# Optimization experiments

Hardware: AMD Instinct MI355X
Metric: run time of the kernel (lower is better)

The kernel has to match this reference:

```python
import jax, jax.numpy as jnp
import numpy as np
from jax import lax

BN_EPS = 1e-5


def _batchnorm(x, gamma, beta):
    # training-mode BatchNorm2d: batch stats over (B, T, J), biased variance
    mean = jnp.mean(x, axis=(0, 2, 3), keepdims=True)
    var = jnp.var(x, axis=(0, 2, 3), keepdims=True)
    inv = lax.rsqrt(var + BN_EPS)
    return (x - mean) * inv * gamma[None, :, None, None] + beta[None, :, None, None]


def setup_inputs() -> dict:
    key = jax.random.key(0)
    ks = jax.random.split(key, 6)
    B, C, T, J = 32, 64, 300, 25
    Cout, K = 64, 9
    x = jax.random.normal(ks[0], (B, C, T, J), dtype=jnp.float32)
    A = jax.random.uniform(ks[1], (J, J), dtype=jnp.float32)
    gcn_w = jax.random.normal(ks[2], (Cout, C), dtype=jnp.float32) * (1.0 / np.sqrt(C))
    gcn_b = jax.random.normal(ks[3], (Cout,), dtype=jnp.float32) * 0.01
    tcn_w = jax.random.normal(ks[4], (Cout, Cout, K, 1), dtype=jnp.float32) * (1.0 / np.sqrt(Cout * K))
    tcn_b = jax.random.normal(ks[5], (Cout,), dtype=jnp.float32) * 0.01
    return {
        "x": x, "A": A,
        "gcn_w": gcn_w, "gcn_b": gcn_b,
        "bn1_g": jnp.ones((Cout,), jnp.float32), "bn1_b": jnp.zeros((Cout,), jnp.float32),
        "tcn_w": tcn_w, "tcn_b": tcn_b,
        "bn2_g": jnp.ones((Cout,), jnp.float32), "bn2_b": jnp.zeros((Cout,), jnp.float32),
    }


def reference(x, A, gcn_w, gcn_b, bn1_g, bn1_b, tcn_w, tcn_b, bn2_g, bn2_b):
    # x: [B, C, T, J]; A: [J, J]
    res = x  # identity residual (in_channels == out_channels, stride == 1)
    # spatial graph conv: joint mixing then 1x1 channel mix (Conv2d k=1)
    y = jnp.einsum('bctj,jk->bctk', x, A)
    y = jnp.einsum('bctj,oc->botj', y, gcn_w) + gcn_b[None, :, None, None]
    y = _batchnorm(y, bn1_g, bn1_b)
    # temporal conv: ReLU -> Conv2d((K,1), pad (K//2,0)) -> BN
    y = jax.nn.relu(y)
    K = tcn_w.shape[2]
    y = lax.conv_general_dilated(
        y, tcn_w, window_strides=(1, 1), padding=((K // 2, K // 2), (0, 0)),
        dimension_numbers=('NCHW', 'OIHW', 'NCHW'))
    y = y + tcn_b[None, :, None, None]
    y = _batchnorm(y, bn2_g, bn2_b)
    return jax.nn.relu(y + res)
```

## Files before the change

kernel.cpp:

```cpp
#include <hip/hip_runtime.h>

#define B_   32
#define C_   64
#define T_   300
#define J_   25
#define K9   9
constexpr int PLANE = T_ * J_;
constexpr int BCTJ  = B_ * C_ * PLANE;
constexpr float BN_EPS = 1e-5f;
constexpr float BN_N   = (float)(B_ * T_ * J_);

typedef __attribute__((ext_vector_type(8))) _Float16 f16x8;
typedef __attribute__((ext_vector_type(2))) _Float16 f16x2;
typedef __attribute__((ext_vector_type(4))) float f32x4;
typedef __attribute__((ext_vector_type(8))) unsigned short u16x8;
typedef __attribute__((ext_vector_type(4))) unsigned short u16x4;

__device__ inline unsigned short f2h(float f) {
  _Float16 h = (_Float16)f;
  return __builtin_bit_cast(unsigned short, h);
}
__device__ inline float h2f(unsigned short u) {
  return (float)__builtin_bit_cast(_Float16, u);
}

__device__ inline void gload16(const unsigned short* g, unsigned short* l) {
  __builtin_amdgcn_global_load_lds(
      (const __attribute__((address_space(1))) unsigned int*)g,
      (__attribute__((address_space(3))) unsigned int*)l, 16, 0, 0);
}

__global__ __launch_bounds__(256) void prep_kernel(const float* __restrict__ tw,
                                                   const float* __restrict__ gw,
                                                   const float* __restrict__ A,
                                                   unsigned short* __restrict__ Wb,
                                                   unsigned short* __restrict__ Gb,
                                                   unsigned short* __restrict__ AdT) {
  int idx = blockIdx.x * 256 + threadIdx.x;
  if (idx < C_ * C_ * K9) {
    int o = idx / (C_ * K9);
    int rem = idx % (C_ * K9);
    int c = rem / K9, kt = rem % K9;
    Wb[kt * (C_ * C_) + o * C_ + c] = f2h(tw[idx]);
  } else if (idx < C_ * C_ * K9 + C_ * C_) {
    int i = idx - C_ * C_ * K9;
    Gb[i] = f2h(gw[i]);
  } else if (idx < C_ * C_ * K9 + C_ * C_ + 256 * 256) {
    int i = idx - (C_ * C_ * K9 + C_ * C_);
    int n = i >> 8, m = i & 255;
    float v = 0.f;
    if (n < 250 && m < 250) {
      if (n / 25 == m / 25) v = A[(m % 25) * 25 + (n % 25)];
    }
    AdT[i] = f2h(v);
  }
}

constexpr int TTG = 10;
__global__ __launch_bounds__(256, 4) void gcn_mfma_kernel(
    const float* __restrict__ x, const unsigned short* __restrict__ AdT,
    const unsigned short* __restrict__ Gb, const float* __restrict__ gbias,
    unsigned short* __restrict__ y1Tb, float* __restrict__ part1) {
  __shared__ unsigned short Xs[C_ * 256];
  __shared__ float sred[4][64], qred[4][64];
  int bid = (blockIdx.x & 7) * 120 + (blockIdx.x >> 3);
  int b = bid / (T_ / TTG), tile = bid % (T_ / TTG);
  int t0 = tile * TTG;
  int tid = threadIdx.x;

  {
    size_t sbase = (size_t)b * (C_ * PLANE) + (size_t)t0 * J_;
    int c0 = tid >> 6;
    int m  = (tid & 63) * 4;
    float4 vb[16];
#pragma unroll
    for (int k = 0; k < 16; ++k) {
      size_t off = sbase + (size_t)(c0 + 4 * k) * PLANE + m;
      size_t offc = off > (size_t)(BCTJ - 4) ? (size_t)(BCTJ - 4) : off;
      float4 v = *(const float4*)(x + offc);
      if (off != offc) {
        v.x = v.z; v.y = v.w; v.z = 0.f; v.w = 0.f;
      }
      vb[k] = v;
    }
#pragma unroll
    for (int k = 0; k < 16; ++k) {
      int c = c0 + 4 * k;
      unsigned p0 = (unsigned)f2h(vb[k].x) | ((unsigned)f2h(vb[k].y) << 16);
      unsigned p1 = (unsigned)f2h(vb[k].z) | ((unsigned)f2h(vb[k].w) << 16);
      int elem = ((c << 8) | m) ^ ((c & 7) << 3);
      *(uint2*)&Xs[elem] = make_uint2(p0, p1);
    }
  }
  __syncthreads();

  int l = tid & 63, w = tid >> 6;
  int lr = l & 15, lh = l >> 4;
  int n0 = w * 64;

  f32x4 acc1[4][4];
#pragma unroll
  for (int mf = 0; mf < 4; ++mf)
#pragma unroll
    for (int nf = 0; nf < 4; ++nf) acc1[mf][nf] = (f32x4)0.f;

  int qminw = ((n0 / 25) * 25) >> 5;
  int qmaxw = min(7, ((((n0 + 63) / 25) + 1) * 25 - 1) >> 5);
  for (int q = qminw; q <= qmaxw; ++q) {
    f16x8 afx[4];
#pragma unroll
    for (int mf = 0; mf < 4; ++mf) {
      int c = mf * 16 + lr;
      int elem = ((c << 8) | (q * 32 + lh * 8)) ^ ((c & 7) << 3);
      afx[mf] = *(const f16x8*)&Xs[elem];
    }
#pragma unroll
    for (int nf = 0; nf < 4; ++nf) {
      int nbase = n0 + nf * 16;
      int ql = ((nbase / 25) * 25) >> 5;
      int qh = min(7, ((((nbase + 15) / 25) + 1) * 25 - 1) >> 5);
      if (q < ql || q > qh) continue;
      int n = nbase + lr;
      f16x8 bfx = *(const f16x8*)&AdT[n * 256 + q * 32 + lh * 8];
#pragma unroll
      for (int mf = 0; mf < 4; ++mf)
        acc1[mf][nf] = __builtin_amdgcn_mfma_f32_16x16x32_f16(afx[mf], bfx, acc1[mf][nf], 0, 0, 0);
    }
  }
  __syncthreads();

#pragma unroll
  for (int mf = 0; mf < 4; ++mf) {
    int cb = mf * 16 + 4 * lh;
#pragma unroll
    for (int nf = 0; nf < 4; ++nf) {
      int n = n0 + nf * 16 + lr;
      unsigned p0 = (unsigned)f2h(acc1[mf][nf][0]) | ((unsigned)f2h(acc1[mf][nf][1]) << 16);
      unsigned p1 = (unsigned)f2h(acc1[mf][nf][2]) | ((unsigned)f2h(acc1[mf][nf][3]) << 16);
      int e0 = ((n << 6) | cb) ^ ((n & 7) << 3);
      *(uint2*)&Xs[e0] = make_uint2(p0, p1);
    }
  }
  __syncthreads();

  f32x4 acc[4][4];
#pragma unroll
  for (int mf = 0; mf < 4; ++mf)
#pragma unroll
    for (int nf = 0; nf < 4; ++nf) acc[mf][nf] = (f32x4)0.f;

  f16x8 af[4][2];
#pragma unroll
  for (int mf = 0; mf < 4; ++mf) {
    const unsigned short* wp = Gb + (mf * 16 + lr) * C_ + lh * 8;
    af[mf][0] = *(const f16x8*)(wp);
    af[mf][1] = *(const f16x8*)(wp + 32);
  }
  f16x8 bfr[4][2];
#pragma unroll
  for (int nf = 0; nf < 4; ++nf) {
    int r = n0 + nf * 16 + lr;
    int sw = (r & 7) << 3;
    bfr[nf][0] = *(const f16x8*)&Xs[((r << 6) | (lh * 8)) ^ sw];
    bfr[nf][1] = *(const f16x8*)&Xs[((r << 6) | (32 + lh * 8)) ^ sw];
  }
#pragma unroll
  for (int mf = 0; mf < 4; ++mf)
#pragma unroll
    for (int nf = 0; nf < 4; ++nf) {
      acc[mf][nf] = __builtin_amdgcn_mfma_f32_16x16x32_f16(af[mf][0], bfr[nf][0], acc[mf][nf], 0, 0, 0);
      acc[mf][nf] = __builtin_amdgcn_mfma_f32_16x16x32_f16(af[mf][1], bfr[nf][1], acc[mf][nf], 0, 0, 0);
    }
  __syncthreads();

#pragma unroll
  for (int mf = 0; mf < 4; ++mf) {
    float4 gb4 = *(const float4*)(gbias + mf * 16 + 4 * lh);
    int cb = mf * 16 + 4 * lh;
    float sv[4] = {0.f, 0.f, 0.f, 0.f}, qv[4] = {0.f, 0.f, 0.f, 0.f};
#pragma unroll
    for (int nf = 0; nf < 4; ++nf) {
      int n = n0 + nf * 16 + lr;
      float v0 = acc[mf][nf][0] + gb4.x;
      float v1 = acc[mf][nf][1] + gb4.y;
      float v2 = acc[mf][nf][2] + gb4.z;
      float v3 = acc[mf][nf][3] + gb4.w;
      if (n < 250) {
        sv[0] += v0; qv[0] += v0 * v0;
        sv[1] += v1; qv[1] += v1 * v1;
        sv[2] += v2; qv[2] += v2 * v2;
        sv[3] += v3; qv[3] += v3 * v3;
      }
      unsigned p0 = (unsigned)f2h(v0) | ((unsigned)f2h(v1) << 16);
      unsigned p1 = (unsigned)f2h(v2) | ((unsigned)f2h(v3) << 16);
      int e0 = ((n << 6) | cb) ^ ((n & 7) << 3);
      *(uint2*)&Xs[e0] = make_uint2(p0, p1);
    }
#pragma unroll
    for (int reg = 0; reg < 4; ++reg) {
      float s = sv[reg], q = qv[reg];
#pragma unroll
      for (int m = 1; m < 16; m <<= 1) {
        s += __shfl_xor(s, m);
        q += __shfl_xor(q, m);
      }
      if (lr == 0) {
        int o = mf * 16 + 4 * lh + reg;
        sred[w][o] = s; qred[w][o] = q;
      }
    }
  }
  __syncthreads();

  unsigned short* ydst = y1Tb + ((size_t)b * PLANE + (size_t)t0 * J_) * C_;
#pragma unroll
  for (int it = 0; it < 8; ++it) {
    int task = it * 256 + tid;
    int n = task >> 3, ch = task & 7;
    if (n < 250) {
      int e = ((n << 6) | (ch * 8)) ^ ((n & 7) << 3);
      u16x8 v = *(const u16x8*)&Xs[e];
      *(u16x8*)(ydst + (size_t)n * C_ + ch * 8) = v;
    }
  }
  if (tid < 64) {
    float S = 0.f, Q = 0.f;
#pragma unroll
    for (int i = 0; i < 4; ++i) { S += sred[i][tid]; Q += qred[i][tid]; }
    part1[bid * 128 + tid] = S;
    part1[bid * 128 + 64 + tid] = Q;
  }
}

__global__ __launch_bounds__(256) void bnparam_reduce_kernel(
    const float* __restrict__ part, int nparts,
    const float* __restrict__ g, const float* __restrict__ b,
    float* __restrict__ bnp, unsigned short* __restrict__ bnph) {
  int c = blockIdx.x;
  int tid = threadIdx.x;
  float S = 0.f, Q = 0.f;
  for (int k = tid; k < nparts; k += 256) {
    S += part[k * 128 + c];
    Q += part[k * 128 + 64 + c];
  }
#pragma unroll
  for (int off = 32; off > 0; off >>= 1) {
    S += __shfl_down(S, off);
    Q += __shfl_down(Q, off);
  }
  __shared__ float ls[2][4];
  int wv = tid >> 6, ln = tid & 63;
  if (ln == 0) { ls[0][wv] = S; ls[1][wv] = Q; }
  __syncthreads();
  if (tid == 0) {
    float St = ls[0][0] + ls[0][1] + ls[0][2] + ls[0][3];
    float Qt = ls[1][0] + ls[1][1] + ls[1][2] + ls[1][3];
    float mean = St / BN_N;
    float var = Qt / BN_N - mean * mean;
    float inv = rsqrtf(var + BN_EPS);
    float sc = g[c] * inv;
    float sh = b[c] - mean * sc;
    bnp[c] = sc;
    bnp[C_ + c] = sh;
    bnph[c] = f2h(sc);
    bnph[C_ + c] = f2h(sh);
  }
}

constexpr int TT = 10;
constexpr int ZROWS_TOT = 456;
__global__ __launch_bounds__(256, 2) void tcn_mfma_kernel(
    const unsigned short* __restrict__ y1Tb, const unsigned short* __restrict__ Wb,
    const unsigned short* __restrict__ bnph1, const float* __restrict__ tbias,
    unsigned short* __restrict__ y2b, float* __restrict__ part2) {
  __shared__ unsigned short zs[ZROWS_TOT * C_];
  __shared__ float sred[4][64], qred[4][64];
  unsigned short* zs2 = zs;
  int bid = (blockIdx.x & 7) * 120 + (blockIdx.x >> 3);
  int b = bid / (T_ / TT), tile = bid % (T_ / TT);
  int t0 = tile * TT;
  int tid = threadIdx.x;
  int g0 = t0 * J_ - 100;

  {
    const unsigned short* bb = y1Tb + (size_t)b * PLANE * C_;
#pragma unroll
    for (int k = 0; k < 15; ++k) {
      int P = k * 256 + tid;
      if (P < 3600) {
        int r = P >> 3, p = P & 7;
        int gr = g0 + r;
        int grc = min(max(gr, 0), PLANE - 1);
        const unsigned short* src = bb + (size_t)grc * C_ + ((p ^ (r & 7)) << 3);
        int ldsoff = (k * 256 + (tid & 192)) << 4;
        gload16(src, (unsigned short*)((char*)zs + ldsoff));
      }
    }
  }

  int l = tid & 63, w = tid >> 6;
  int lr = l & 15, lh = l >> 4;
  int n0 = w * 64;

  f16x2 scA[4], shA[4], scB[4], shB[4];
  {
    const f16x2* scp = (const f16x2*)(bnph1);
    const f16x2* shp = (const f16x2*)(bnph1 + C_);
#pragma unroll
    for (int i = 0; i < 4; ++i) {
      scA[i] = scp[lh * 4 + i];      shA[i] = shp[lh * 4 + i];
      scB[i] = scp[16 + lh * 4 + i]; shB[i] = shp[16 + lh * 4 + i];
    }
  }
  f16x2 z2 = (f16x2)((_Float16)0.f);

  f32x4 acc[4][4];
#pragma unroll
  for (int mf = 0; mf < 4; ++mf)
#pragma unroll
    for (int nf = 0; nf < 4; ++nf) acc[mf][nf] = (f32x4)0.f;

  f16x8 afc[4][2];
#pragma unroll
  for (int mf = 0; mf < 4; ++mf) {
    const unsigned short* wp = Wb + (mf * 16 + lr) * C_ + lh * 8;
    afc[mf][0] = *(const f16x8*)(wp);
    afc[mf][1] = *(const f16x8*)(wp + 32);
  }
  __syncthreads();

  auto load_bfr = [&](int kt, f16x8 out[4][2]) {
#pragma unroll
    for (int nf = 0; nf < 4; ++nf) {
      int r = n0 + nf * 16 + lr + 25 * kt;
      int gr = g0 + r;
      int sw = (r & 7) << 3;
      uint4 ra = *(const uint4*)&zs[((r << 6) | (lh * 8)) ^ sw];
      uint4 rb = *(const uint4*)&zs[((r << 6) | (32 + lh * 8)) ^ sw];
      f16x2 a0 = __builtin_bit_cast(f16x2, ra.x);
      f16x2 a1 = __builtin_bit_cast(f16x2, ra.y);
      f16x2 a2 = __builtin_bit_cast(f16x2, ra.z);
      f16x2 a3 = __builtin_bit_cast(f16x2, ra.w);
      f16x2 b0 = __builtin_bit_cast(f16x2, rb.x);
      f16x2 b1 = __builtin_bit_cast(f16x2, rb.y);
      f16x2 b2 = __builtin_bit_cast(f16x2, rb.z);
      f16x2 b3 = __builtin_bit_cast(f16x2, rb.w);
      a0 = __builtin_elementwise_max(a0 * scA[0] + shA[0], z2);
      a1 = __builtin_elementwise_max(a1 * scA[1] + shA[1], z2);
      a2 = __builtin_elementwise_max(a2 * scA[2] + shA[2], z2);
      a3 = __builtin_elementwise_max(a3 * scA[3] + shA[3], z2);
      b0 = __builtin_elementwise_max(b0 * scB[0] + shB[0], z2);
      b1 = __builtin_elementwise_max(b1 * scB[1] + shB[1], z2);
      b2 = __builtin_elementwise_max(b2 * scB[2] + shB[2], z2);
      b3 = __builtin_elementwise_max(b3 * scB[3] + shB[3], z2);
      unsigned m = ((unsigned)gr < (unsigned)PLANE && r < 450) ? 0xFFFFFFFFu : 0u;
      uint4 pa, pb;
      pa.x = __builtin_bit_cast(unsigned int, a0) & m;
      pa.y = __builtin_bit_cast(unsigned int, a1) & m;
      pa.z = __builtin_bit_cast(unsigned int, a2) & m;
      pa.w = __builtin_bit_cast(unsigned int, a3) & m;
      pb.x = __builtin_bit_cast(unsigned int, b0) & m;
      pb.y = __builtin_bit_cast(unsigned int, b1) & m;
      pb.z = __builtin_bit_cast(unsigned int, b2) & m;
      pb.w = __builtin_bit_cast(unsigned int, b3) & m;
      out[nf][0] = __builtin_bit_cast(f16x8, pa);
      out[nf][1] = __builtin_bit_cast(f16x8, pb);
    }
  };

  f16x8 bcur[4][2], bnxt[4][2];
  load_bfr(0, bcur);

#pragma unroll
  for (int kt = 0; kt < K9; ++kt) {
    f16x8 afn[4][2];
    if (kt < K9 - 1) {
#pragma unroll
      for (int mf = 0; mf < 4; ++mf) {
        const unsigned short* wp = Wb + (kt + 1) * (C_ * C_) + (mf * 16 + lr) * C_ + lh * 8;
        afn[mf][0] = *(const f16x8*)(wp);
        afn[mf][1] = *(const f16x8*)(wp + 32);
      }
      load_bfr(kt + 1, bnxt);
    }
    __builtin_amdgcn_s_setprio(1);
#pragma unroll
    for (int mf = 0; mf < 4; ++mf)
#pragma unroll
      for (int nf = 0; nf < 4; ++nf) {
        acc[mf][nf] = __builtin_amdgcn_mfma_f32_16x16x32_f16(afc[mf][0], bcur[nf][0], acc[mf][nf], 0, 0, 0);
        acc[mf][nf] = __builtin_amdgcn_mfma_f32_16x16x32_f16(afc[mf][1], bcur[nf][1], acc[mf][nf], 0, 0, 0);
      }
    __builtin_amdgcn_s_setprio(0);
    if (kt < K9 - 1) {
#pragma unroll
      for (int mf = 0; mf < 4; ++mf) {
        afc[mf][0] = afn[mf][0];
        afc[mf][1] = afn[mf][1];
      }
#pragma unroll
      for (int nf = 0; nf < 4; ++nf) {
        bcur[nf][0] = bnxt[nf][0];
        bcur[nf][1] = bnxt[nf][1];
      }
    }
  }
  __syncthreads();

#pragma unroll
  for (int mf = 0; mf < 4; ++mf) {
    float4 tb4 = *(const float4*)(tbias + mf * 16 + 4 * lh);
    float sv[4] = {0.f, 0.f, 0.f, 0.f}, qv[4] = {0.f, 0.f, 0.f, 0.f};
#pragma unroll
    for (int nf = 0; nf < 4; ++nf) {
      int n = n0 + nf * 16 + lr;
      if (n < 250) {
#pragma unroll
        for (int reg = 0; reg < 4; ++reg) {
          int o = mf * 16 + 4 * lh + reg;
          float v = acc[mf][nf][reg] + ((const float*)&tb4)[reg];
          zs2[o * 260 + n] = f2h(v);
          sv[reg] += v; qv[reg] += v * v;
        }
      }
    }
#pragma unroll
    for (int reg = 0; reg < 4; ++reg) {
      float s = sv[reg], q = qv[reg];
#pragma unroll
      for (int m = 1; m < 16; m <<= 1) {
        s += __shfl_xor(s, m);
        q += __shfl_xor(q, m);
      }
      if (lr == 0) {
        int o = mf * 16 + 4 * lh + reg;
        sred[w][o] = s; qred[w][o] = q;
      }
    }
  }
  __syncthreads();

  unsigned short* ydst = y2b + (size_t)b * (C_ * PLANE) + (size_t)t0 * J_;
#pragma unroll
  for (int it = 0; it < 32; ++it) {
    int task = it * 256 + tid;
    if (task < 8000) {
      int o = task / 125;
      int k = task - o * 125;
      unsigned d = *(const unsigned*)&zs2[o * 260 + 2 * k];
      *(unsigned*)(ydst + (size_t)o * PLANE + 2 * k) = d;
    }
  }
  if (tid < 64) {
    float S = 0.f, Q = 0.f;
#pragma unroll
    for (int i = 0; i < 4; ++i) { S += sred[i][tid]; Q += qred[i][tid]; }
    part2[bid * 128 + tid] = S;
    part2[bid * 128 + 64 + tid] = Q;
  }
}

__global__ __launch_bounds__(256) void final_kernel(const unsigned short* __restrict__ y2b,
                                                    const float* __restrict__ x,
                                                    const float* __restrict__ bnp2,
                                                    float* __restrict__ out) {
  int lb = (blockIdx.x & 7) * 1875 + (blockIdx.x >> 3);
  int i = lb * 256 + threadIdx.x;
  if (i >= BCTJ / 4) return;
  int c = (i / (PLANE / 4)) & (C_ - 1);
  float sc = bnp2[c], sh = bnp2[C_ + c];
  u16x4 yv = *(const u16x4*)(y2b + (size_t)i * 4);
  float4 xv = ((const float4*)x)[i];
  float4 v;
  v.x = fmaxf(fmaf(h2f(yv[0]), sc, sh) + xv.x, 0.f);
  v.y = fmaxf(fmaf(h2f(yv[1]), sc, sh) + xv.y, 0.f);
  v.z = fmaxf(fmaf(h2f(yv[2]), sc, sh) + xv.z, 0.f);
  v.w = fmaxf(fmaf(h2f(yv[3]), sc, sh) + xv.w, 0.f);
  ((float4*)out)[i] = v;
}

extern "C" void kernel_launch(void* const* d_in, const int* in_sizes, int n_in,
                              void* d_out, int out_size, void* d_ws, size_t ws_size,
                              hipStream_t stream) {
  const float* x     = (const float*)d_in[0];
  const float* A     = (const float*)d_in[1];
  const float* gcn_w = (const float*)d_in[2];
  const float* gcn_b = (const float*)d_in[3];
  const float* bn1_g = (const float*)d_in[4];
  const float* bn1_b = (const float*)d_in[5];
  const float* tcn_w = (const float*)d_in[6];
  const float* tcn_b = (const float*)d_in[7];
  const float* bn2_g = (const float*)d_in[8];
  const float* bn2_b = (const float*)d_in[9];
  float* out = (float*)d_out;

  unsigned short* y1Tb = (unsigned short*)d_ws;
  unsigned short* y2b  = y1Tb + BCTJ;
  unsigned short* Wb   = y2b + BCTJ;
  unsigned short* Gb   = Wb + C_ * C_ * K9;
  unsigned short* AdT  = Gb + C_ * C_;
  unsigned short* bnph = AdT + 256 * 256;
  float* part = (float*)(bnph + 256);
  float* bnp  = part + 960 * 128;

  int prep_n = C_ * C_ * K9 + C_ * C_ + 256 * 256;
  prep_kernel<<<(prep_n + 255) / 256, 256, 0, stream>>>(tcn_w, gcn_w, A, Wb, Gb, AdT);
  gcn_mfma_kernel<<<B_ * (T_ / TTG), 256, 0, stream>>>(x, AdT, Gb, gcn_b, y1Tb, part);
  bnparam_reduce_kernel<<<64, 256, 0, stream>>>(part, B_ * (T_ / TTG), bn1_g, bn1_b, bnp, bnph);
  tcn_mfma_kernel<<<B_ * (T_ / TT), 256, 0, stream>>>(y1Tb, Wb, bnph, tcn_b, y2b, part);
  bnparam_reduce_kernel<<<64, 256, 0, stream>>>(part, B_ * (T_ / TT), bn2_g, bn2_b, bnp + 128, bnph + 128);
  final_kernel<<<BCTJ / 4 / 256, 256, 0, stream>>>(y2b, x, bnp + 128, out);
}
```

Before: 118.2 us.

## Tile temporal conv per (batch, joint) and store intermediate channel-last with transposing final kernel

The temporal conv kernel now processes one full time sequence per (batch, joint) block, 800 blocks, instead of 10-timestep tiles spanning all joints. This cuts the halo rows loaded per block and shrinks LDS so three blocks fit per CU. The per-k B-fragment prefetch is dropped, and the intermediate is written channel-last through a padded LDS tile. The final kernel now transposes that layout through shared memory back to NCHW before the BN, residual and ReLU step. The trade-offs are gathered 128-byte row loads with stride J*C, uneven work across waves, and an extra LDS transpose in the final pass.

```diff
diff --git a/kernel.cpp b/kernel.cpp
--- a/kernel.cpp
+++ b/kernel.cpp
@@ -267,31 +267,28 @@
   }
 }
 
-constexpr int TT = 10;
-constexpr int ZROWS_TOT = 456;
-__global__ __launch_bounds__(256, 2) void tcn_mfma_kernel(
+constexpr int ZRJ = 312;
+__global__ __launch_bounds__(256, 3) void tcn_mfma_kernel(
     const unsigned short* __restrict__ y1Tb, const unsigned short* __restrict__ Wb,
     const unsigned short* __restrict__ bnph1, const float* __restrict__ tbias,
-    unsigned short* __restrict__ y2b, float* __restrict__ part2) {
-  __shared__ unsigned short zs[ZROWS_TOT * C_];
+    unsigned short* __restrict__ y2T, float* __restrict__ part2) {
+  __shared__ __align__(16) unsigned short zsU[304 * 72];
   __shared__ float sred[4][64], qred[4][64];
-  unsigned short* zs2 = zs;
-  int bid = (blockIdx.x & 7) * 120 + (blockIdx.x >> 3);
-  int b = bid / (T_ / TT), tile = bid % (T_ / TT);
-  int t0 = tile * TT;
+  unsigned short* zs  = zsU;
+  unsigned short* zs2 = zsU;
+  int bid = (blockIdx.x & 7) * 100 + (blockIdx.x >> 3);
+  int b = bid / J_, j = bid % J_;
   int tid = threadIdx.x;
-  int g0 = t0 * J_ - 100;
 
   {
     const unsigned short* bb = y1Tb + (size_t)b * PLANE * C_;
 #pragma unroll
-    for (int k = 0; k < 15; ++k) {
+    for (int k = 0; k < 10; ++k) {
       int P = k * 256 + tid;
-      if (P < 3600) {
+      if (P < ZRJ * 8) {
         int r = P >> 3, p = P & 7;
-        int gr = g0 + r;
-        int grc = min(max(gr, 0), PLANE - 1);
-        const unsigned short* src = bb + (size_t)grc * C_ + ((p ^ (r & 7)) << 3);
+        int tc = min(max(r - 4, 0), T_ - 1);
+        const unsigned short* src = bb + (size_t)(tc * J_ + j) * C_ + ((p ^ (r & 7)) << 3);
         int ldsoff = (k * 256 + (tid & 192)) << 4;
         gload16(src, (unsigned short*)((char*)zs + ldsoff));
       }
@@ -300,7 +297,8 @@
 
   int l = tid & 63, w = tid >> 6;
   int lr = l & 15, lh = l >> 4;
-  int n0 = w * 64;
+  int n0 = w * 80;
+  int nfmax = (w < 3) ? 5 : 4;
 
   f16x2 scA[4], shA[4], scB[4], shB[4];
   {
@@ -314,11 +312,11 @@
   }
   f16x2 z2 = (f16x2)((_Float16)0.f);
 
-  f32x4 acc[4][4];
+  f32x4 acc[4][5];
 #pragma unroll
   for (int mf = 0; mf < 4; ++mf)
 #pragma unroll
-    for (int nf = 0; nf < 4; ++nf) acc[mf][nf] = (f32x4)0.f;
+    for (int nf = 0; nf < 5; ++nf) acc[mf][nf] = (f32x4)0.f;
 
   f16x8 afc[4][2];
 #pragma unroll
@@ -329,11 +327,22 @@
   }
   __syncthreads();
 
-  auto load_bfr = [&](int kt, f16x8 out[4][2]) {
-#pragma unroll
-    for (int nf = 0; nf < 4; ++nf) {
-      int r = n0 + nf * 16 + lr + 25 * kt;
-      int gr = g0 + r;
+#pragma unroll
+  for (int kt = 0; kt < K9; ++kt) {
+    f16x8 afn[4][2];
+    if (kt < K9 - 1) {
+#pragma unroll
+      for (int mf = 0; mf < 4; ++mf) {
+        const unsigned short* wp = Wb + (kt + 1) * (C_ * C_) + (mf * 16 + lr) * C_ + lh * 8;
+        afn[mf][0] = *(const f16x8*)(wp);
+        afn[mf][1] = *(const f16x8*)(wp + 32);
+      }
+    }
+    f16x8 bfr[5][2];
+#pragma unroll
+    for (int nf = 0; nf < 5; ++nf) {
+      if (nf >= nfmax) continue;
+      int r = n0 + nf * 16 + lr + kt;
       int sw = (r & 7) << 3;
       uint4 ra = *(const uint4*)&zs[((r << 6) | (lh * 8)) ^ sw];
       uint4 rb = *(const uint4*)&zs[((r << 6) | (32 + lh * 8)) ^ sw];
@@ -353,7 +362,7 @@
       b1 = __builtin_elementwise_max(b1 * scB[1] + shB[1], z2);
       b2 = __builtin_elementwise_max(b2 * scB[2] + shB[2], z2);
       b3 = __builtin_elementwise_max(b3 * scB[3] + shB[3], z2);
-      unsigned m = ((unsigned)gr < (unsigned)PLANE && r < 450) ? 0xFFFFFFFFu : 0u;
+      unsigned m = ((unsigned)(r - 4) < (unsigned)T_) ? 0xFFFFFFFFu : 0u;
       uint4 pa, pb;
       pa.x = __builtin_bit_cast(unsigned int, a0) & m;
       pa.y = __builtin_bit_cast(unsigned int, a1) & m;
@@ -363,33 +372,17 @@
       pb.y = __builtin_bit_cast(unsigned int, b1) & m;
       pb.z = __builtin_bit_cast(unsigned int, b2) & m;
       pb.w = __builtin_bit_cast(unsigned int, b3) & m;
-      out[nf][0] = __builtin_bit_cast(f16x8, pa);
-      out[nf][1] = __builtin_bit_cast(f16x8, pb);
-    }
-  };
-
-  f16x8 bcur[4][2], bnxt[4][2];
-  load_bfr(0, bcur);
-
-#pragma unroll
-  for (int kt = 0; kt < K9; ++kt) {
-    f16x8 afn[4][2];
-    if (kt < K9 - 1) {
-#pragma unroll
-      for (int mf = 0; mf < 4; ++mf) {
-        const unsigned short* wp = Wb + (kt + 1) * (C_ * C_) + (mf * 16 + lr) * C_ + lh * 8;
-        afn[mf][0] = *(const f16x8*)(wp);
-        afn[mf][1] = *(const f16x8*)(wp + 32);
-      }
-      load_bfr(kt + 1, bnxt);
+      bfr[nf][0] = __builtin_bit_cast(f16x8, pa);
+      bfr[nf][1] = __builtin_bit_cast(f16x8, pb);
     }
     __builtin_amdgcn_s_setprio(1);
 #pragma unroll
     for (int mf = 0; mf < 4; ++mf)
 #pragma unroll
-      for (int nf = 0; nf < 4; ++nf) {
-        acc[mf][nf] = __builtin_amdgcn_mfma_f32_16x16x32_f16(afc[mf][0], bcur[nf][0], acc[mf][nf], 0, 0, 0);
-        acc[mf][nf] = __builtin_amdgcn_mfma_f32_16x16x32_f16(afc[mf][1], bcur[nf][1], acc[mf][nf], 0, 0, 0);
+      for (int nf = 0; nf < 5; ++nf) {
+        if (nf >= nfmax) continue;
+        acc[mf][nf] = __builtin_amdgcn_mfma_f32_16x16x32_f16(afc[mf][0], bfr[nf][0], acc[mf][nf], 0, 0, 0);
+        acc[mf][nf] = __builtin_amdgcn_mfma_f32_16x16x32_f16(afc[mf][1], bfr[nf][1], acc[mf][nf], 0, 0, 0);
       }
     __builtin_amdgcn_s_setprio(0);
     if (kt < K9 - 1) {
@@ -398,11 +391,6 @@
         afc[mf][0] = afn[mf][0];
         afc[mf][1] = afn[mf][1];
       }
-#pragma unroll
-      for (int nf = 0; nf < 4; ++nf) {
-        bcur[nf][0] = bnxt[nf][0];
-        bcur[nf][1] = bnxt[nf][1];
-      }
     }
   }
   __syncthreads();
@@ -412,16 +400,21 @@
     float4 tb4 = *(const float4*)(tbias + mf * 16 + 4 * lh);
     float sv[4] = {0.f, 0.f, 0.f, 0.f}, qv[4] = {0.f, 0.f, 0.f, 0.f};
 #pragma unroll
-    for (int nf = 0; nf < 4; ++nf) {
-      int n = n0 + nf * 16 + lr;
-      if (n < 250) {
-#pragma unroll
-        for (int reg = 0; reg < 4; ++reg) {
-          int o = mf * 16 + 4 * lh + reg;
-          float v = acc[mf][nf][reg] + ((const float*)&tb4)[reg];
-          zs2[o * 260 + n] = f2h(v);
-          sv[reg] += v; qv[reg] += v * v;
-        }
+    for (int nf = 0; nf < 5; ++nf) {
+      if (nf >= nfmax) continue;
+      int t = n0 + nf * 16 + lr;
+      if (t < T_) {
+        float v0 = acc[mf][nf][0] + tb4.x;
+        float v1 = acc[mf][nf][1] + tb4.y;
+        float v2 = acc[mf][nf][2] + tb4.z;
+        float v3 = acc[mf][nf][3] + tb4.w;
+        sv[0] += v0; qv[0] += v0 * v0;
+        sv[1] += v1; qv[1] += v1 * v1;
+        sv[2] += v2; qv[2] += v2 * v2;
+        sv[3] += v3; qv[3] += v3 * v3;
+        unsigned p0 = (unsigned)f2h(v0) | ((unsigned)f2h(v1) << 16);
+        unsigned p1 = (unsigned)f2h(v2) | ((unsigned)f2h(v3) << 16);
+        *(uint2*)&zs2[t * 72 + mf * 16 + 4 * lh] = make_uint2(p0, p1);
       }
     }
 #pragma unroll
@@ -440,15 +433,14 @@
   }
   __syncthreads();
 
-  unsigned short* ydst = y2b + (size_t)b * (C_ * PLANE) + (size_t)t0 * J_;
-#pragma unroll
-  for (int it = 0; it < 32; ++it) {
+  unsigned short* ydst = y2T + ((size_t)b * PLANE + j) * C_;
+#pragma unroll
+  for (int it = 0; it < 10; ++it) {
     int task = it * 256 + tid;
-    if (task < 8000) {
-      int o = task / 125;
-      int k = task - o * 125;
-      unsigned d = *(const unsigned*)&zs2[o * 260 + 2 * k];
-      *(unsigned*)(ydst + (size_t)o * PLANE + 2 * k) = d;
+    if (task < T_ * 8) {
+      int t = task >> 3, ch = task & 7;
+      u16x8 v = *(const u16x8*)&zs2[t * 72 + ch * 8];
+      *(u16x8*)(ydst + (size_t)t * (J_ * C_) + ch * 8) = v;
     }
   }
   if (tid < 64) {
@@ -460,23 +452,47 @@
   }
 }
 
-__global__ __launch_bounds__(256) void final_kernel(const unsigned short* __restrict__ y2b,
-                                                    const float* __restrict__ x,
-                                                    const float* __restrict__ bnp2,
-                                                    float* __restrict__ out) {
-  int lb = (blockIdx.x & 7) * 1875 + (blockIdx.x >> 3);
-  int i = lb * 256 + threadIdx.x;
-  if (i >= BCTJ / 4) return;
-  int c = (i / (PLANE / 4)) & (C_ - 1);
-  float sc = bnp2[c], sh = bnp2[C_ + c];
-  u16x4 yv = *(const u16x4*)(y2b + (size_t)i * 4);
-  float4 xv = ((const float4*)x)[i];
-  float4 v;
-  v.x = fmaxf(fmaf(h2f(yv[0]), sc, sh) + xv.x, 0.f);
-  v.y = fmaxf(fmaf(h2f(yv[1]), sc, sh) + xv.y, 0.f);
-  v.z = fmaxf(fmaf(h2f(yv[2]), sc, sh) + xv.z, 0.f);
-  v.w = fmaxf(fmaf(h2f(yv[3]), sc, sh) + xv.w, 0.f);
-  ((float4*)out)[i] = v;
+constexpr int FR = 64;
+constexpr int NCH = (PLANE + FR - 1) / FR;
+__global__ __launch_bounds__(256) void final_kernel(
+    const unsigned short* __restrict__ y2T, const float* __restrict__ x,
+    const float* __restrict__ bnp2, float* __restrict__ out) {
+  __shared__ float zt[FR][65];
+  int lb = (blockIdx.x & 7) * (B_ * NCH / 8) + (blockIdx.x >> 3);
+  int b = lb / NCH, ch = lb % NCH;
+  int r0 = ch * FR;
+  int rem = min(FR, PLANE - r0);
+  int tid = threadIdx.x;
+  {
+    int c8 = (tid & 7) * 8;
+    const unsigned short* src = y2T + ((size_t)b * PLANE + r0) * C_ + c8;
+#pragma unroll
+    for (int k = 0; k < 2; ++k) {
+      int r = (tid >> 3) + k * 32;
+      if (r < rem) {
+        u16x8 v = *(const u16x8*)(src + (size_t)r * C_);
+#pragma unroll
+        for (int i = 0; i < 8; ++i) zt[r][c8 + i] = h2f(v[i]);
+      }
+    }
+  }
+  __syncthreads();
+  int pos = (tid & 31) * 2;
+  int cs = tid >> 5;
+#pragma unroll
+  for (int pass = 0; pass < 8; ++pass) {
+    int c = pass * 8 + cs;
+    if (pos < rem) {
+      float sc = bnp2[c], sh = bnp2[C_ + c];
+      size_t gi = (size_t)(b * C_ + c) * PLANE + r0 + pos;
+      float z0 = zt[pos][c], z1 = zt[pos + 1][c];
+      float2 xv = *(const float2*)(x + gi);
+      float2 o2;
+      o2.x = fmaxf(fmaf(z0, sc, sh) + xv.x, 0.f);
+      o2.y = fmaxf(fmaf(z1, sc, sh) + xv.y, 0.f);
+      *(float2*)(out + gi) = o2;
+    }
+  }
 }
 
 extern "C" void kernel_launch(void* const* d_in, const int* in_sizes, int n_in,
@@ -495,8 +511,8 @@
   float* out = (float*)d_out;
 
   unsigned short* y1Tb = (unsigned short*)d_ws;
-  unsigned short* y2b  = y1Tb + BCTJ;
-  unsigned short* Wb   = y2b + BCTJ;
+  unsigned short* y2T  = y1Tb + BCTJ;
+  unsigned short* Wb   = y2T + BCTJ;
   unsigned short* Gb   = Wb + C_ * C_ * K9;
   unsigned short* AdT  = Gb + C_ * C_;
   unsigned short* bnph = AdT + 256 * 256;
@@ -507,7 +523,7 @@
   prep_kernel<<<(prep_n + 255) / 256, 256, 0, stream>>>(tcn_w, gcn_w, A, Wb, Gb, AdT);
   gcn_mfma_kernel<<<B_ * (T_ / TTG), 256, 0, stream>>>(x, AdT, Gb, gcn_b, y1Tb, part);
   bnparam_reduce_kernel<<<64, 256, 0, stream>>>(part, B_ * (T_ / TTG), bn1_g, bn1_b, bnp, bnph);
-  tcn_mfma_kernel<<<B_ * (T_ / TT), 256, 0, stream>>>(y1Tb, Wb, bnph, tcn_b, y2b, part);
-  bnparam_reduce_kernel<<<64, 256, 0, stream>>>(part, B_ * (T_ / TT), bn2_g, bn2_b, bnp + 128, bnph + 128);
-  final_kernel<<<BCTJ / 4 / 256, 256, 0, stream>>>(y2b, x, bnp + 128, out);
-}
+  tcn_mfma_kernel<<<B_ * J_, 256, 0, stream>>>(y1Tb, Wb, bnph, tcn_b, y2T, part);
+  bnparam_reduce_kernel<<<64, 256, 0, stream>>>(part, B_ * J_, bn2_g, bn2_b, bnp + 128, bnph + 128);
+  final_kernel<<<B_ * NCH, 256, 0, stream>>>(y2T, x, bnp + 128, out);
+}
```

After: 209.1 us. +76.9%, slower.
